# Performance work log

Measured on AMD Instinct MI355X. Metric: run time of the kernel, lower is better.

## Reference

```python
import jax, jax.numpy as jnp
import numpy as np

# NF4 codebook used by bitsandbytes (16 levels, normalized to [-1, 1])
NF4_CODE = jnp.array([
    -1.0, -0.6961928009986877, -0.5250730514526367, -0.39491748809814453,
    -0.28444138169288635, -0.18477343022823334, -0.09105003625154495, 0.0,
    0.07958029955625534, 0.16093020141124725, 0.24611230194568634,
    0.33791524171829224, 0.44070982933044434, 0.5626170039176941,
    0.7229568362236023, 1.0], dtype=jnp.float32)
BLOCKSIZE = 64  # bitsandbytes default 4-bit blocksize


def nf4_quant_dequant(w):
    """Simulate bnb NF4 quantize -> dequantize (per-block absmax scaling)."""
    shape = w.shape
    flat = w.reshape(-1, BLOCKSIZE)                     # [n_blocks, 64]
    absmax = jnp.max(jnp.abs(flat), axis=1, keepdims=True)
    normalized = flat / jnp.where(absmax == 0, 1.0, absmax)
    # nearest-codebook-value quantization via midpoint boundaries
    bounds = (NF4_CODE[:-1] + NF4_CODE[1:]) * 0.5       # [15]
    idx = jnp.searchsorted(bounds, normalized)          # [n_blocks, 64] in [0,15]
    return (NF4_CODE[idx] * absmax).reshape(shape)


def setup_inputs() -> dict:
    key = jax.random.key(0)
    k1, k2, k3, kx = jax.random.split(key, 4)
    D, H = 4096, 11008
    scale = 0.02  # typical transformer init scale
    w1 = jax.random.normal(k1, (H, D), jnp.float32) * scale
    w2 = jax.random.normal(k2, (H, D), jnp.float32) * scale
    w3 = jax.random.normal(k3, (D, H), jnp.float32) * scale
    x = jax.random.normal(kx, (2, 2048, D), jnp.float32)
    return {"x": x, "w1": w1, "w2": w2, "w3": w3}


def reference(x, w1, w2, w3):
    dq1 = nf4_quant_dequant(w1)   # [H, D]
    dq2 = nf4_quant_dequant(w2)   # [H, D]
    dq3 = nf4_quant_dequant(w3)   # [D, H]
    gate = jnp.einsum('bsd,hd->bsh', x, dq1)
    up = jnp.einsum('bsd,hd->bsh', x, dq2)
    h = jax.nn.silu(gate) * up
    return jnp.einsum('bsh,dh->bsd', h, dq3)
```

## Files before the change

kernel.cpp:

```cpp
#include <hip/hip_runtime.h>
#include <math.h>

typedef __attribute__((ext_vector_type(4))) float f32x4;
typedef __attribute__((ext_vector_type(8))) short bf16x8;

#define DI __device__ __forceinline__

DI unsigned short f32_to_bf16(float f) {
  unsigned int u = __float_as_uint(f);
  u += 0x7FFFu + ((u >> 16) & 1u);
  return (unsigned short)(u >> 16);
}

static constexpr float kCode[16] = {
    -1.0f, -0.6961928009986877f, -0.5250730514526367f, -0.39491748809814453f,
    -0.28444138169288635f, -0.18477343022823334f, -0.09105003625154495f, 0.0f,
    0.07958029955625534f, 0.16093020141124725f, 0.24611230194568634f,
    0.33791524171829224f, 0.44070982933044434f, 0.5626170039176941f,
    0.7229568362236023f, 1.0f};

DI void dequant_body(const float* __restrict__ in, unsigned short* __restrict__ out, int i) {
  f32x4 v = reinterpret_cast<const f32x4*>(in)[i];
  float am = fmaxf(fmaxf(fabsf(v.x), fabsf(v.y)), fmaxf(fabsf(v.z), fabsf(v.w)));
  am = fmaxf(am, __shfl_xor(am, 1));
  am = fmaxf(am, __shfl_xor(am, 2));
  am = fmaxf(am, __shfl_xor(am, 4));
  am = fmaxf(am, __shfl_xor(am, 8));
  const float scale = (am == 0.0f) ? 1.0f : am;
  float sb[15];
#pragma unroll
  for (int b = 0; b < 15; ++b)
    sb[b] = (0.5f * (kCode[b] + kCode[b + 1])) * scale;
  unsigned short o[4];
#pragma unroll
  for (int j = 0; j < 4; ++j) {
    const float vj = ((const float*)&v)[j];
    int idx = 0;
#pragma unroll
    for (int b = 0; b < 15; ++b)
      idx += (vj > sb[b]) ? 1 : 0;
    o[j] = f32_to_bf16(kCode[idx] * am);
  }
  reinterpret_cast<ushort4*>(out)[i] = make_ushort4(o[0], o[1], o[2], o[3]);
}

__global__ void __launch_bounds__(256) k_dequant_nf4(
    const float* __restrict__ in, unsigned short* __restrict__ out, int n4) {
  int i = blockIdx.x * 256 + threadIdx.x;
  if (i >= n4) return;
  dequant_body(in, out, i);
}

__global__ void __launch_bounds__(256) k_dequant_nf4_2(
    const float* __restrict__ in1, const float* __restrict__ in2,
    unsigned short* __restrict__ out1, unsigned short* __restrict__ out2, int n4) {
  int i = blockIdx.x * 256 + threadIdx.x;
  if (i < n4) {
    dequant_body(in1, out1, i);
  } else {
    dequant_body(in2, out2, i - n4);
  }
}

__global__ void __launch_bounds__(256) k_f32_to_bf16(
    const float* __restrict__ in, unsigned short* __restrict__ out, int n4) {
  int i = blockIdx.x * 256 + threadIdx.x;
  if (i >= n4) return;
  f32x4 v = reinterpret_cast<const f32x4*>(in)[i];
  reinterpret_cast<ushort4*>(out)[i] =
      make_ushort4(f32_to_bf16(v.x), f32_to_bf16(v.y), f32_to_bf16(v.z), f32_to_bf16(v.w));
}

DI void gload16(const void* g, void* l) {
  __builtin_amdgcn_global_load_lds(
      (const __attribute__((address_space(1))) void*)g,
      (__attribute__((address_space(3))) void*)l, 16, 0, 0);
}

DI void barrier_nodrain() {
  asm volatile("" ::: "memory");
  __builtin_amdgcn_s_barrier();
  asm volatile("" ::: "memory");
}

#define WAITV(N) asm volatile("s_waitcnt vmcnt(" #N ")" ::: "memory")

DI float fast_silu(float g) {
  const float e = __builtin_amdgcn_exp2f(g * -1.442695041f);
  return g * __builtin_amdgcn_rcpf(1.0f + e);
}

__global__ void __launch_bounds__(1024, 4) k_gemm_dual_swiglu(
    const unsigned short* __restrict__ X,
    const unsigned short* __restrict__ W1,
    const unsigned short* __restrict__ W2,
    unsigned short* __restrict__ H) {
  constexpr int K = 4096, N = 11008, NK = K / 32;
  __shared__ char ldsb[131072];

  const int tid = threadIdx.x;
  const int w = tid >> 6, l = tid & 63;

  const int bid = blockIdx.x;
  const int xcd = bid & 7, ii = bid >> 3;
  const int nt = ii >> 1;
  const int mt = xcd * 2 + (ii & 1);
  const int m0 = mt * 256, n0 = nt * 128;

  const int p = w & 7;
  const bool isGate = (w < 8);
  const int wr = p >> 1, wc = p & 1;

  const int lrow = l >> 2;
  const int kc8 = (((l & 3) ^ ((l >> 3) & 3)) << 3);
  const unsigned short* gsrc0;
  const unsigned short* gsrc1;
  int ldst0;
  if (w < 8) {
    gsrc0 = X + (size_t)(m0 + 32 * w + lrow) * K + kc8;
    gsrc1 = X + (size_t)(m0 + 32 * w + 16 + lrow) * K + kc8;
    ldst0 = 2 * w * 1024;
  } else if (w < 12) {
    gsrc0 = W1 + (size_t)(n0 + 32 * (w - 8) + lrow) * K + kc8;
    gsrc1 = W1 + (size_t)(n0 + 32 * (w - 8) + 16 + lrow) * K + kc8;
    ldst0 = 16384 + (w - 8) * 2048;
  } else {
    gsrc0 = W2 + (size_t)(n0 + 32 * (w - 12) + lrow) * K + kc8;
    gsrc1 = W2 + (size_t)(n0 + 32 * (w - 12) + 16 + lrow) * K + kc8;
    ldst0 = 24576 + (w - 12) * 2048;
  }

  const int roff = (((l >> 4) ^ ((l >> 1) & 3)) << 4);
  const char* rdA = ldsb + (wr * 64 + (l & 15)) * 64 + roff;
  const char* rdB = ldsb + 16384 + (isGate ? 0 : 8192) +
                    (wc * 64 + (l & 15)) * 64 + roff;

  f32x4 acc[4][4] = {};

#define TILE_BODY(bo) {                                                        \
  bf16x8 a[4], b[4];                                                           \
  _Pragma("unroll") for (int m = 0; m < 4; ++m)                                \
    a[m] = *(const bf16x8*)(rdA + (bo) + m * 1024);                            \
  _Pragma("unroll") for (int n = 0; n < 4; ++n)                                \
    b[n] = *(const bf16x8*)(rdB + (bo) + n * 1024);                            \
  __builtin_amdgcn_s_setprio(1);                                               \
  _Pragma("unroll") for (int m = 0; m < 4; ++m)                                \
    _Pragma("unroll") for (int n = 0; n < 4; ++n)                              \
      acc[m][n] = __builtin_amdgcn_mfma_f32_16x16x32_bf16(a[m], b[n], acc[m][n], 0, 0, 0); \
  __builtin_amdgcn_s_setprio(0); }

  gload16(gsrc0, ldsb + ldst0);               gload16(gsrc1, ldsb + ldst0 + 1024);
  gload16(gsrc0 + 32, ldsb + 32768 + ldst0);  gload16(gsrc1 + 32, ldsb + 32768 + ldst0 + 1024);
  gload16(gsrc0 + 64, ldsb + 65536 + ldst0);  gload16(gsrc1 + 64, ldsb + 65536 + ldst0 + 1024);
  const unsigned short* pg0 = gsrc0 + 96;
  const unsigned short* pg1 = gsrc1 + 96;
  WAITV(4);
  barrier_nodrain();

  int t = 0;
  for (; t + 3 < NK; ++t) {
    const int bo = (t & 3) << 15;
    const int bs = ((t + 3) & 3) << 15;
    gload16(pg0, ldsb + bs + ldst0);
    gload16(pg1, ldsb + bs + ldst0 + 1024);
    pg0 += 32; pg1 += 32;
    TILE_BODY(bo);
    WAITV(4); barrier_nodrain();
  }
  TILE_BODY((t & 3) << 15); WAITV(2); barrier_nodrain(); ++t;
  TILE_BODY((t & 3) << 15); WAITV(0); barrier_nodrain(); ++t;
  TILE_BODY((t & 3) << 15);
#undef TILE_BODY

  barrier_nodrain();
  char* xch = ldsb + p * 16384 + (isGate ? 0 : 8192);
#pragma unroll
  for (int m2 = 0; m2 < 2; ++m2)
#pragma unroll
    for (int n = 0; n < 4; ++n) {
      const int m = isGate ? (m2 + 2) : m2;
      *(f32x4*)(xch + ((m2 * 4 + n) * 64 + l) * 16) = acc[m][n];
    }
  barrier_nodrain();
  const char* oxch = ldsb + p * 16384 + (isGate ? 8192 : 0);
  const int er = (l >> 4) * 4, ec = l & 15;
#pragma unroll
  for (int m2 = 0; m2 < 2; ++m2)
#pragma unroll
    for (int n = 0; n < 4; ++n) {
      const int mk = isGate ? m2 : (m2 + 2);
      f32x4 other = *(const f32x4*)(oxch + ((m2 * 4 + n) * 64 + l) * 16);
#pragma unroll
      for (int j = 0; j < 4; ++j) {
        const float g_ = isGate ? acc[mk][n][j] : other[j];
        const float u_ = isGate ? other[j] : acc[mk][n][j];
        const float s = fast_silu(g_);
        const int row = m0 + wr * 64 + mk * 16 + er + j;
        const int col = n0 + wc * 64 + n * 16 + ec;
        H[(size_t)row * N + col] = f32_to_bf16(s * u_);
      }
    }
}

__global__ void __launch_bounds__(1024, 4) k_gemm_out(
    const unsigned short* __restrict__ Hm,
    const unsigned short* __restrict__ W3,
    float* __restrict__ Out) {
  constexpr int K = 11008, N = 4096, NK = K / 32;
  __shared__ char ldsb[131072];

  const int tid = threadIdx.x;
  const int w = tid >> 6, l = tid & 63;

  const int bid = blockIdx.x;
  const int xcd = bid & 7, ii = bid >> 3;
  const int nt = ii >> 1;
  const int mt = xcd * 2 + (ii & 1);
  const int m0 = mt * 256, n0 = nt * 256;

  const int wr = w >> 2, wc = w & 3;

  const int lrow = l >> 2;
  const int kc8 = (((l & 3) ^ ((l >> 3) & 3)) << 3);
  const unsigned short* gsrc0;
  const unsigned short* gsrc1;
  int ldst0;
  if (w < 8) {
    gsrc0 = Hm + (size_t)(m0 + 32 * w + lrow) * K + kc8;
    gsrc1 = Hm + (size_t)(m0 + 32 * w + 16 + lrow) * K + kc8;
    ldst0 = 2 * w * 1024;
  } else {
    gsrc0 = W3 + (size_t)(n0 + 32 * (w - 8) + lrow) * K + kc8;
    gsrc1 = W3 + (size_t)(n0 + 32 * (w - 8) + 16 + lrow) * K + kc8;
    ldst0 = 16384 + (w - 8) * 2048;
  }

  const int roff = (((l >> 4) ^ ((l >> 1) & 3)) << 4);
  const char* rdA = ldsb + (wr * 64 + (l & 15)) * 64 + roff;
  const char* rdB = ldsb + 16384 + (wc * 64 + (l & 15)) * 64 + roff;

  f32x4 acc[4][4] = {};

#define TILE_BODY(bo) {                                                        \
  bf16x8 a[4], b[4];                                                           \
  _Pragma("unroll") for (int m = 0; m < 4; ++m)                                \
    a[m] = *(const bf16x8*)(rdA + (bo) + m * 1024);                            \
  _Pragma("unroll") for (int n = 0; n < 4; ++n)                                \
    b[n] = *(const bf16x8*)(rdB + (bo) + n * 1024);                            \
  __builtin_amdgcn_s_setprio(1);                                               \
  _Pragma("unroll") for (int m = 0; m < 4; ++m)                                \
    _Pragma("unroll") for (int n = 0; n < 4; ++n)                              \
      acc[m][n] = __builtin_amdgcn_mfma_f32_16x16x32_bf16(a[m], b[n], acc[m][n], 0, 0, 0); \
  __builtin_amdgcn_s_setprio(0); }

  gload16(gsrc0, ldsb + ldst0);               gload16(gsrc1, ldsb + ldst0 + 1024);
  gload16(gsrc0 + 32, ldsb + 32768 + ldst0);  gload16(gsrc1 + 32, ldsb + 32768 + ldst0 + 1024);
  gload16(gsrc0 + 64, ldsb + 65536 + ldst0);  gload16(gsrc1 + 64, ldsb + 65536 + ldst0 + 1024);
  const unsigned short* pg0 = gsrc0 + 96;
  const unsigned short* pg1 = gsrc1 + 96;
  WAITV(4);
  barrier_nodrain();

  int t = 0;
  for (; t + 3 < NK; ++t) {
    const int bo = (t & 3) << 15;
    const int bs = ((t + 3) & 3) << 15;
    gload16(pg0, ldsb + bs + ldst0);
    gload16(pg1, ldsb + bs + ldst0 + 1024);
    pg0 += 32; pg1 += 32;
    TILE_BODY(bo);
    WAITV(4); barrier_nodrain();
  }
  TILE_BODY((t & 3) << 15); WAITV(2); barrier_nodrain(); ++t;
  TILE_BODY((t & 3) << 15); WAITV(0); barrier_nodrain(); ++t;
  TILE_BODY((t & 3) << 15);
#undef TILE_BODY

  const int er = (l >> 4) * 4, ec = l & 15;
#pragma unroll
  for (int m = 0; m < 4; ++m)
#pragma unroll
    for (int n = 0; n < 4; ++n) {
      const int row = m0 + wr * 64 + m * 16 + er;
      const int col = n0 + wc * 64 + n * 16 + ec;
      float* ptr = Out + (size_t)row * N + col;
#pragma unroll
      for (int j = 0; j < 4; ++j) ptr[(size_t)j * N] = acc[m][n][j];
    }
}

extern "C" void kernel_launch(void* const* d_in, const int* in_sizes, int n_in,
                              void* d_out, int out_size, void* d_ws, size_t ws_size,
                              hipStream_t stream) {
  const float* x  = (const float*)d_in[0];
  const float* w1 = (const float*)d_in[1];
  const float* w2 = (const float*)d_in[2];
  const float* w3 = (const float*)d_in[3];
  float* out = (float*)d_out;

  char* ws = (char*)d_ws;
  unsigned short* xb  = (unsigned short*)(ws);
  unsigned short* w1b = (unsigned short*)(ws + 33554432);
  unsigned short* w2b = (unsigned short*)(ws + 123731968);
  unsigned short* hb  = (unsigned short*)(ws + 213909504);
  unsigned short* w3b = w1b;

  const int NW = 11008 * 4096 / 4;
  k_f32_to_bf16<<<16384, 256, 0, stream>>>(x, xb, 4096 * 4096 / 4);
  k_dequant_nf4_2<<<2 * (NW / 256), 256, 0, stream>>>(w1, w2, w1b, w2b, NW);

  k_gemm_dual_swiglu<<<1376, 1024, 0, stream>>>(xb, w1b, w2b, hb);

  k_dequant_nf4<<<NW / 256, 256, 0, stream>>>(w3, w3b, NW);

  k_gemm_out<<<256, 1024, 0, stream>>>(hb, w3b, out);
}
```

Measured before the change: 1.216 ms.

## Use five-stage LDS ring and process two K-tiles per barrier in both GEMMs

Both GEMM kernels grow the shared-memory ring from four 32KB stages to five (160KB). The main loop now issues loads for two K-tiles at once and computes two tiles between barriers, halving the number of block-wide barriers and waits. The cost is more LDS per block, which relies on the MI355X's larger LDS, plus more complex prologue/epilogue offset bookkeeping with a wrap helper.

```diff
diff --git a/kernel.cpp b/kernel.cpp
--- a/kernel.cpp
+++ b/kernel.cpp
@@ -90,13 +90,15 @@
   return g * __builtin_amdgcn_rcpf(1.0f + e);
 }
 
+DI int wrap5(int x) { return x >= 163840 ? x - 163840 : x; }
+
 __global__ void __launch_bounds__(1024, 4) k_gemm_dual_swiglu(
     const unsigned short* __restrict__ X,
     const unsigned short* __restrict__ W1,
     const unsigned short* __restrict__ W2,
     unsigned short* __restrict__ H) {
   constexpr int K = 4096, N = 11008, NK = K / 32;
-  __shared__ char ldsb[131072];
+  __shared__ char ldsb[163840];
 
   const int tid = threadIdx.x;
   const int w = tid >> 6, l = tid & 63;
@@ -154,22 +156,34 @@
   gload16(gsrc0 + 64, ldsb + 65536 + ldst0);  gload16(gsrc1 + 64, ldsb + 65536 + ldst0 + 1024);
   const unsigned short* pg0 = gsrc0 + 96;
   const unsigned short* pg1 = gsrc1 + 96;
-  WAITV(4);
+  WAITV(2);
   barrier_nodrain();
 
-  int t = 0;
-  for (; t + 3 < NK; ++t) {
-    const int bo = (t & 3) << 15;
-    const int bs = ((t + 3) & 3) << 15;
-    gload16(pg0, ldsb + bs + ldst0);
-    gload16(pg1, ldsb + bs + ldst0 + 1024);
-    pg0 += 32; pg1 += 32;
-    TILE_BODY(bo);
-    WAITV(4); barrier_nodrain();
-  }
-  TILE_BODY((t & 3) << 15); WAITV(2); barrier_nodrain(); ++t;
-  TILE_BODY((t & 3) << 15); WAITV(0); barrier_nodrain(); ++t;
-  TILE_BODY((t & 3) << 15);
+  int bo_r0 = 0, bo_r1 = 32768;
+  int bo_s0 = 98304, bo_s1 = 131072;
+  for (int t = 0; t + 4 < NK; t += 2) {
+    gload16(pg0, ldsb + bo_s0 + ldst0);
+    gload16(pg1, ldsb + bo_s0 + ldst0 + 1024);
+    gload16(pg0 + 32, ldsb + bo_s1 + ldst0);
+    gload16(pg1 + 32, ldsb + bo_s1 + ldst0 + 1024);
+    pg0 += 64; pg1 += 64;
+    TILE_BODY(bo_r0);
+    __builtin_amdgcn_sched_barrier(0);
+    TILE_BODY(bo_r1);
+    WAITV(2); barrier_nodrain();
+    bo_r0 = wrap5(bo_r0 + 65536); bo_r1 = wrap5(bo_r1 + 65536);
+    bo_s0 = wrap5(bo_s0 + 65536); bo_s1 = wrap5(bo_s1 + 65536);
+  }
+  gload16(pg0, ldsb + bo_s0 + ldst0);
+  gload16(pg1, ldsb + bo_s0 + ldst0 + 1024);
+  TILE_BODY(bo_r0);
+  __builtin_amdgcn_sched_barrier(0);
+  TILE_BODY(bo_r1);
+  WAITV(0); barrier_nodrain();
+  bo_r0 = wrap5(bo_r0 + 65536); bo_r1 = wrap5(bo_r1 + 65536);
+  TILE_BODY(bo_r0);
+  __builtin_amdgcn_sched_barrier(0);
+  TILE_BODY(bo_r1);
 #undef TILE_BODY
 
   barrier_nodrain();
@@ -207,7 +221,7 @@
     const unsigned short* __restrict__ W3,
     float* __restrict__ Out) {
   constexpr int K = 11008, N = 4096, NK = K / 32;
-  __shared__ char ldsb[131072];
+  __shared__ char ldsb[163840];
 
   const int tid = threadIdx.x;
   const int w = tid >> 6, l = tid & 63;
@@ -258,22 +272,34 @@
   gload16(gsrc0 + 64, ldsb + 65536 + ldst0);  gload16(gsrc1 + 64, ldsb + 65536 + ldst0 + 1024);
   const unsigned short* pg0 = gsrc0 + 96;
   const unsigned short* pg1 = gsrc1 + 96;
-  WAITV(4);
+  WAITV(2);
   barrier_nodrain();
 
-  int t = 0;
-  for (; t + 3 < NK; ++t) {
-    const int bo = (t & 3) << 15;
-    const int bs = ((t + 3) & 3) << 15;
-    gload16(pg0, ldsb + bs + ldst0);
-    gload16(pg1, ldsb + bs + ldst0 + 1024);
-    pg0 += 32; pg1 += 32;
-    TILE_BODY(bo);
-    WAITV(4); barrier_nodrain();
-  }
-  TILE_BODY((t & 3) << 15); WAITV(2); barrier_nodrain(); ++t;
-  TILE_BODY((t & 3) << 15); WAITV(0); barrier_nodrain(); ++t;
-  TILE_BODY((t & 3) << 15);
+  int bo_r0 = 0, bo_r1 = 32768;
+  int bo_s0 = 98304, bo_s1 = 131072;
+  for (int t = 0; t + 4 < NK; t += 2) {
+    gload16(pg0, ldsb + bo_s0 + ldst0);
+    gload16(pg1, ldsb + bo_s0 + ldst0 + 1024);
+    gload16(pg0 + 32, ldsb + bo_s1 + ldst0);
+    gload16(pg1 + 32, ldsb + bo_s1 + ldst0 + 1024);
+    pg0 += 64; pg1 += 64;
+    TILE_BODY(bo_r0);
+    __builtin_amdgcn_sched_barrier(0);
+    TILE_BODY(bo_r1);
+    WAITV(2); barrier_nodrain();
+    bo_r0 = wrap5(bo_r0 + 65536); bo_r1 = wrap5(bo_r1 + 65536);
+    bo_s0 = wrap5(bo_s0 + 65536); bo_s1 = wrap5(bo_s1 + 65536);
+  }
+  gload16(pg0, ldsb + bo_s0 + ldst0);
+  gload16(pg1, ldsb + bo_s0 + ldst0 + 1024);
+  TILE_BODY(bo_r0);
+  __builtin_amdgcn_sched_barrier(0);
+  TILE_BODY(bo_r1);
+  WAITV(0); barrier_nodrain();
+  bo_r0 = wrap5(bo_r0 + 65536); bo_r1 = wrap5(bo_r1 + 65536);
+  TILE_BODY(bo_r0);
+  __builtin_amdgcn_sched_barrier(0);
+  TILE_BODY(bo_r1);
 #undef TILE_BODY
 
   const int er = (l >> 4) * 4, ec = l & 15;
```

After: 1.251 ms. +2.8%, slower.
